# Kernel optimization log

Measured on AMD Instinct MI355X. Metric: run time of the kernel, lower is better.

The kernel has to match this reference:

```python
import jax, jax.numpy as jnp
import numpy as np

B, N, D, E = 4, 1024, 1024, 8
TOP_N = 2
THRESHOLD = 0.2
EPS = 1e-9
CAP_FACTOR = 2.0
MIN_EXPERT_CAPACITY = 4
H = int(D * 4 * 2 / 3)  # GEGLU hidden = 2730


def setup_inputs() -> dict:
    key = jax.random.key(0)
    ks = jax.random.split(key, 8)
    u = lambda k, shape, fan: jax.random.uniform(k, shape, jnp.float32, -1.0, 1.0) * (fan ** -0.5)
    return {
        "x": jax.random.normal(ks[0], (B, N, D), jnp.float32),
        "route_probs": jax.random.uniform(ks[1], (TOP_N, B, N), jnp.float32),
        "gate_w": u(ks[2], (D, E), D),
        "w1": u(ks[3], (E, D, 2 * H), 2 * H),
        "b1": u(ks[4], (E, 2 * H), 2 * H),
        "mult_bias": jnp.ones((E, H), jnp.float32),
        "w2": u(ks[5], (E, H, D), D),
        "b2": u(ks[6], (E, D), D),
    }


def reference(x, route_probs, gate_w, w1, b1, mult_bias, w2, b2):
    b, n, d = x.shape
    e = gate_w.shape[1]
    cap = max(min(n, int(n * CAP_FACTOR / e)), MIN_EXPERT_CAPACITY)  # 256

    # ---- top-n gating ----
    logits = jnp.einsum('bnd,de->bne', x, gate_w)
    raw_gates = jax.nn.softmax(logits, axis=-1)
    gate_vals, gate_idx = jax.lax.top_k(raw_gates, TOP_N)          # [b,n,k]
    gate_vals = jnp.moveaxis(gate_vals, -1, 0)                      # [k,b,n]
    gate_idx = jnp.moveaxis(gate_idx, -1, 0)                        # [k,b,n]
    one_hot_idx = jax.nn.one_hot(gate_idx, e, dtype=x.dtype)        # [k,b,n,e]

    denom = jnp.clip(gate_vals.sum(axis=0, keepdims=True), EPS)
    gate_vals = gate_vals / denom

    # route to expert k>0 with prob min(1, gate/threshold); expert 0 always routed
    should_route = route_probs < (gate_vals / THRESHOLD)
    should_route = should_route.at[0].set(True)
    mask = one_hot_idx * should_route[..., None].astype(x.dtype)    # [k,b,n,e]

    # exclusive cumsum over sequence dim -> position within each expert
    mask_cumsum = jnp.cumsum(mask, axis=2) - mask                   # [k,b,n,e]

    positions, masks = [], []
    prev_count = jnp.zeros((b, 1, e), x.dtype)
    for k in range(TOP_N):  # small fixed loop over top-n
        pos_e = (mask_cumsum[k] + prev_count) * mask[k]             # [b,n,e]
        mk = mask[k] * (pos_e < float(cap)).astype(x.dtype)
        prev_count = prev_count + mk.sum(axis=1, keepdims=True)
        positions.append(pos_e.sum(axis=-1))                        # [b,n]
        masks.append(mk)
    positions = jnp.stack(positions)                                # [k,b,n]
    mask = jnp.stack(masks)                                         # [k,b,n,e]

    mask_flat = mask.sum(axis=-1)                                   # [k,b,n] in {0,1}
    gates = gate_vals * mask_flat
    pos_one_hot = jax.nn.one_hot(positions.astype(jnp.int32), cap, dtype=x.dtype)  # [k,b,n,c]

    # combine tensor [b,n,e,c]; dispatch is its boolean support
    combine = jnp.einsum('kbn,kbne,kbnc->bnec', gates * mask_flat, one_hot_idx, pos_one_hot)
    dispatch = (combine > 0).astype(x.dtype)

    # ---- dispatch tokens to experts ----
    xe = jnp.einsum('bnd,bnec->ebcd', x, dispatch)                  # [e,b,c,d]

    # ---- per-expert GEGLU FFN (grouped GEMM) ----
    h = jnp.einsum('ebcd,edf->ebcf', xe, w1) + b1[:, None, None, :]
    val, gate = jnp.split(h, 2, axis=-1)
    act = jax.nn.gelu(gate, approximate=False) * val * mult_bias[:, None, None, :]
    out_e = jnp.einsum('ebch,ehd->ebcd', act, w2) + b2[:, None, None, :]

    # ---- combine ----
    out = jnp.einsum('ebcd,bnec->bnd', out_e, combine)
    return out


if __name__ == '__main__':
    inp = setup_inputs()
    o = reference(**inp)
    print(o.shape, o.dtype)
```

## Files before the change

kernel.cpp:

```cpp
#include <hip/hip_runtime.h>
#include <hip/hip_bf16.h>
#include <math.h>

#define B_ 4
#define N_ 1024
#define D_ 1024
#define E_ 8
#define H_ 2730
#define H2_ 5460
#define CAP_ 256
#define NTOK 4096
#define NSLOT 8192
#define NKT1 16
#define NKT2 43
#define NFG 22

typedef __attribute__((ext_vector_type(8))) short short8;
typedef __attribute__((ext_vector_type(4))) float f32x4;

__device__ __forceinline__ unsigned short f2bf(float f) {
    __hip_bfloat16 h = __float2bfloat16(f);
    return *reinterpret_cast<unsigned short*>(&h);
}
__device__ __forceinline__ float bf2f(unsigned short u) {
    unsigned x = ((unsigned)u) << 16;
    union { unsigned u; float f; } c; c.u = x; return c.f;
}

#define GLL16(g, l)                                                          \
    __builtin_amdgcn_global_load_lds(                                        \
        (const __attribute__((address_space(1))) void*)(g),                  \
        (__attribute__((address_space(3))) void*)(l), 16, 0, 0)

#define VMCNT4() asm volatile("s_waitcnt vmcnt(4)" ::: "memory")
#define VMCNT3() asm volatile("s_waitcnt vmcnt(3)" ::: "memory")
#define VMCNT0() asm volatile("s_waitcnt vmcnt(0)" ::: "memory")
#define SBAR()   __builtin_amdgcn_s_barrier()
#define SCHEDB() __builtin_amdgcn_sched_barrier(0)
#define MFMA16(a, b, c) __builtin_amdgcn_mfma_f32_16x16x32_bf16((a), (b), (c), 0, 0, 0)


__global__ __launch_bounds__(256) void k_cvt1(const float* __restrict__ w1,
                                              unsigned short* __restrict__ w1p) {
    const int fg = blockIdx.x;
    const int kt = blockIdx.y;
    const int e  = blockIdx.z;
    const float* w1e = w1 + (size_t)e * D_ * H2_;
    unsigned short* dst = w1p + (((size_t)((e * NFG + fg) * NKT1 + kt)) << 14);
    __shared__ unsigned short tile[128][66];
    const int t = threadIdx.x;
    const int fl4 = (t & 31) * 4;
    const int kr  = t >> 5;
    const int fbase = fg * 128;

    for (int m = 0; m < 2; ++m) {
        if (m) __syncthreads();
        const int c0 = m * H_;
#pragma unroll
        for (int ii = 0; ii < 8; ++ii) {
            const int kl = ii * 8 + kr;
            const float* src = w1e + (size_t)(kt * 64 + kl) * H2_ + c0 + fbase + fl4;
            float v0, v1, v2, v3;
            if (fbase + fl4 + 3 < H_) {
                const float4 v = *reinterpret_cast<const float4*>(src);
                v0 = v.x; v1 = v.y; v2 = v.z; v3 = v.w;
            } else {
                v0 = (fbase + fl4 + 0 < H_) ? src[0] : 0.f;
                v1 = (fbase + fl4 + 1 < H_) ? src[1] : 0.f;
                v2 = (fbase + fl4 + 2 < H_) ? src[2] : 0.f;
                v3 = (fbase + fl4 + 3 < H_) ? src[3] : 0.f;
            }
            tile[fl4 + 0][kl] = f2bf(v0);
            tile[fl4 + 1][kl] = f2bf(v1);
            tile[fl4 + 2][kl] = f2bf(v2);
            tile[fl4 + 3][kl] = f2bf(v3);
        }
        __syncthreads();
#pragma unroll
        for (int i = 0; i < 4; ++i) {
            const int o = i * 256 + t;
            const int k32  = o >> 9;
            const int flhi = (o >> 6) & 7;
            const int lane = o & 63;
            const int kq   = lane >> 4;
            const int fl   = flhi * 16 + (lane & 15);
            const int kb   = k32 * 32 + kq * 8;
            const unsigned* rp = reinterpret_cast<const unsigned*>(&tile[fl][kb]);
            uint4 q; q.x = rp[0]; q.y = rp[1]; q.z = rp[2]; q.w = rp[3];
            const size_t off = ((size_t)k32 << 13) + (size_t)(m * 8 + flhi) * 512 + (size_t)lane * 8;
            *reinterpret_cast<uint4*>(dst + off) = q;
        }
    }
}

__global__ __launch_bounds__(256) void k_cvt2(const float* __restrict__ w2,
                                              unsigned short* __restrict__ w2p) {
    const int kt = blockIdx.x;
    const int nt = blockIdx.y;
    const int e  = blockIdx.z;
    const float* w2e = w2 + (size_t)e * H_ * D_;
    unsigned short* dst = w2p + (((size_t)((e * 8 + nt) * NKT2 + kt)) << 13);
    __shared__ unsigned short tile[128][66];
    const int t = threadIdx.x;
    const int d4 = (t & 31) * 4;
    const int fr = t >> 5;

#pragma unroll
    for (int ii = 0; ii < 8; ++ii) {
        const int fl = ii * 8 + fr;
        const int f = kt * 64 + fl;
        float v0 = 0.f, v1 = 0.f, v2 = 0.f, v3 = 0.f;
        if (f < H_) {
            const float4 v = *reinterpret_cast<const float4*>(w2e + (size_t)f * D_ + nt * 128 + d4);
            v0 = v.x; v1 = v.y; v2 = v.z; v3 = v.w;
        }
        tile[d4 + 0][fl] = f2bf(v0);
        tile[d4 + 1][fl] = f2bf(v1);
        tile[d4 + 2][fl] = f2bf(v2);
        tile[d4 + 3][fl] = f2bf(v3);
    }
    __syncthreads();
#pragma unroll
    for (int i = 0; i < 4; ++i) {
        const int o = i * 256 + t;
        const int k32 = o >> 9;
        const int dhi = (o >> 6) & 7;
        const int lane = o & 63;
        const int kq = lane >> 4;
        const int dl = dhi * 16 + (lane & 15);
        const int fb = k32 * 32 + kq * 8;
        const unsigned* rp = reinterpret_cast<const unsigned*>(&tile[dl][fb]);
        uint4 q; q.x = rp[0]; q.y = rp[1]; q.z = rp[2]; q.w = rp[3];
        const size_t off = ((size_t)k32 << 12) + (size_t)dhi * 512 + (size_t)lane * 8;
        *reinterpret_cast<uint4*>(dst + off) = q;
    }
}

__global__ __launch_bounds__(256) void k_gate(const float* __restrict__ x,
                                              const float* __restrict__ route,
                                              const float* __restrict__ gw,
                                              int* __restrict__ tokE,
                                              float* __restrict__ tokG,
                                              int* __restrict__ tokR) {
    const int wave = threadIdx.x >> 6, lane = threadIdx.x & 63;
    const int t = blockIdx.x * 4 + wave;
    float acc[E_];
#pragma unroll
    for (int e = 0; e < E_; ++e) acc[e] = 0.f;
    const float* xr = x + (size_t)t * D_;
    for (int d = lane; d < D_; d += 64) {
        float xv = xr[d];
        const float* g = gw + d * E_;
#pragma unroll
        for (int e = 0; e < E_; ++e) acc[e] = fmaf(xv, g[e], acc[e]);
    }
#pragma unroll
    for (int e = 0; e < E_; ++e) {
#pragma unroll
        for (int off = 32; off; off >>= 1) acc[e] += __shfl_xor(acc[e], off);
    }
    if (lane == 0) {
        float m = acc[0];
#pragma unroll
        for (int e = 1; e < E_; ++e) m = fmaxf(m, acc[e]);
        float p[E_]; float s = 0.f;
#pragma unroll
        for (int e = 0; e < E_; ++e) { p[e] = expf(acc[e] - m); s += p[e]; }
        int i0 = 0; float v0 = p[0];
#pragma unroll
        for (int e = 1; e < E_; ++e) if (p[e] > v0) { v0 = p[e]; i0 = e; }
        int i1 = (i0 == 0) ? 1 : 0; float v1 = p[i1];
#pragma unroll
        for (int e = 0; e < E_; ++e) if (e != i0 && p[e] > v1) { v1 = p[e]; i1 = e; }
        float p0 = v0 / s, p1 = v1 / s;
        float denom = fmaxf(p0 + p1, 1e-9f);
        float g0 = p0 / denom, g1 = p1 / denom;
        int r1 = route[NTOK + t] < (g1 / 0.2f);
        tokE[t] = i0; tokE[NTOK + t] = i1;
        tokG[t] = g0; tokG[NTOK + t] = g1;
        tokR[t] = r1;
    }
}

__global__ __launch_bounds__(256) void k_pos(const int* __restrict__ tokE,
                                             const float* __restrict__ tokG,
                                             const int* __restrict__ tokR,
                                             int* __restrict__ sot,
                                             int* __restrict__ tos) {
    const int e = blockIdx.x & 7, b = blockIdx.x >> 3;
    const int t = threadIdx.x;
    __shared__ int sc[256];
    const int base_bt = b * N_ + t * 4;
    int m0[4], m1[4];
    int c0 = 0, c1 = 0;
#pragma unroll
    for (int i = 0; i < 4; ++i) {
        int bt = base_bt + i;
        m0[i] = (tokE[bt] == e) ? 1 : 0;
        m1[i] = ((tokE[NTOK + bt] == e) && tokR[bt]) ? 1 : 0;
        c0 += m0[i]; c1 += m1[i];
    }
    int packed = c0 | (c1 << 16);
    sc[t] = packed;
    __syncthreads();
    for (int off = 1; off < 256; off <<= 1) {
        int v = (t >= off) ? sc[t - off] : 0;
        __syncthreads();
        sc[t] += v;
        __syncthreads();
    }
    int incl = sc[t];
    int total = sc[255];
    int excl = incl - packed;
    int base0 = excl & 0xffff;
    int base1 = excl >> 16;
    int kept0 = min(total & 0xffff, CAP_);
#pragma unroll
    for (int i = 0; i < 4; ++i) {
        int bt = base_bt + i;
        if (m0[i]) {
            int pos = base0++;
            if (pos < CAP_ && tokG[bt] > 0.f) {
                int s = ((e * B_ + b) << 8) + pos;
                sot[bt] = s;
                tos[s] = bt;
            }
        }
        if (m1[i]) {
            int pos = (base1++) + kept0;
            if (pos < CAP_ && tokG[NTOK + bt] > 0.f) {
                int s = ((e * B_ + b) << 8) + pos;
                sot[NTOK + bt] = s;
                tos[s] = bt;
            }
        }
    }
}

__global__ __launch_bounds__(256) void k_disp(const float* __restrict__ x,
                                              const int* __restrict__ tos,
                                              unsigned short* __restrict__ xeP) {
    const int t = threadIdx.x;
    const int s = blockIdx.x * 2 + (t >> 7);
    const int q = t & 127;
    const int bt = tos[s];
    const int kt = q >> 3, k32 = (q >> 2) & 1, kq = q & 3;
    const int lane = (kq << 4) | (s & 15);
    const int m16 = (s >> 4) & 15;
    const int sgrp = s >> 8;
    unsigned short* dst = xeP + (((size_t)(sgrp * NKT1 + kt)) << 14) + (k32 << 13) + (m16 << 9) + lane * 8;
    ushort4 r0 = {0, 0, 0, 0}, r1 = {0, 0, 0, 0};
    if (bt >= 0) {
        const float4 v0 = *reinterpret_cast<const float4*>(x + ((size_t)bt << 10) + q * 8);
        const float4 v1 = *reinterpret_cast<const float4*>(x + ((size_t)bt << 10) + q * 8 + 4);
        r0.x = f2bf(v0.x); r0.y = f2bf(v0.y); r0.z = f2bf(v0.z); r0.w = f2bf(v0.w);
        r1.x = f2bf(v1.x); r1.y = f2bf(v1.y); r1.z = f2bf(v1.z); r1.w = f2bf(v1.w);
    }
    *reinterpret_cast<ushort4*>(dst) = r0;
    *reinterpret_cast<ushort4*>(dst + 4) = r1;
}

#define LDF(BUF, idx) (*reinterpret_cast<const short8*>(&BUF[(idx) * 512 + lane8]))

#define FFN1_MM03(AF0, AF1, AF2, AF3)                                         \
    do {                                                                      \
        acc[0][0]=MFMA16(AF0,bf0,acc[0][0]); acc[0][1]=MFMA16(AF0,bf1,acc[0][1]); \
        acc[0][2]=MFMA16(AF0,bf2,acc[0][2]); acc[0][3]=MFMA16(AF0,bf3,acc[0][3]); \
        acc[1][0]=MFMA16(AF1,bf0,acc[1][0]); acc[1][1]=MFMA16(AF1,bf1,acc[1][1]); \
        acc[1][2]=MFMA16(AF1,bf2,acc[1][2]); acc[1][3]=MFMA16(AF1,bf3,acc[1][3]); \
        acc[2][0]=MFMA16(AF2,bf0,acc[2][0]); acc[2][1]=MFMA16(AF2,bf1,acc[2][1]); \
        acc[2][2]=MFMA16(AF2,bf2,acc[2][2]); acc[2][3]=MFMA16(AF2,bf3,acc[2][3]); \
        acc[3][0]=MFMA16(AF3,bf0,acc[3][0]); acc[3][1]=MFMA16(AF3,bf1,acc[3][1]); \
        acc[3][2]=MFMA16(AF3,bf2,acc[3][2]); acc[3][3]=MFMA16(AF3,bf3,acc[3][3]); \
    } while (0)
#define FFN1_MM47(AF0, AF1, AF2, AF3)                                         \
    do {                                                                      \
        acc[4][0]=MFMA16(AF0,bf0,acc[4][0]); acc[4][1]=MFMA16(AF0,bf1,acc[4][1]); \
        acc[4][2]=MFMA16(AF0,bf2,acc[4][2]); acc[4][3]=MFMA16(AF0,bf3,acc[4][3]); \
        acc[5][0]=MFMA16(AF1,bf0,acc[5][0]); acc[5][1]=MFMA16(AF1,bf1,acc[5][1]); \
        acc[5][2]=MFMA16(AF1,bf2,acc[5][2]); acc[5][3]=MFMA16(AF1,bf3,acc[5][3]); \
        acc[6][0]=MFMA16(AF2,bf0,acc[6][0]); acc[6][1]=MFMA16(AF2,bf1,acc[6][1]); \
        acc[6][2]=MFMA16(AF2,bf2,acc[6][2]); acc[6][3]=MFMA16(AF2,bf3,acc[6][3]); \
        acc[7][0]=MFMA16(AF3,bf0,acc[7][0]); acc[7][1]=MFMA16(AF3,bf1,acc[7][1]); \
        acc[7][2]=MFMA16(AF3,bf2,acc[7][2]); acc[7][3]=MFMA16(AF3,bf3,acc[7][3]); \
    } while (0)

#define FFN1_KT(ARD, BRD, AWR, BWR, KTN, PF)                                  \
    do {                                                                      \
        const unsigned short* asn = abase + ((size_t)(KTN) << 14);            \
        const unsigned short* bsn = bbase + ((size_t)(KTN) << 14);            \
        short8 af0, af1, af2, af3, bf0, bf1, bf2, bf3;                        \
        SCHEDB(); VMCNT4(); SBAR(); SCHEDB();                                 \
        if (PF) {                                                             \
            GLL16(asn + woff + lane8, (char*)&AWR[woff]);                     \
            GLL16(asn + woff + 512 + lane8, (char*)&AWR[woff + 512]);         \
        }                                                                     \
        bf0 = LDF(BRD, bn0); bf1 = LDF(BRD, bn0 + 1);                         \
        bf2 = LDF(BRD, bn0 + 8); bf3 = LDF(BRD, bn0 + 9);                     \
        af0 = LDF(ARD, am0 + 0); af1 = LDF(ARD, am0 + 1);                     \
        af2 = LDF(ARD, am0 + 2); af3 = LDF(ARD, am0 + 3);                     \
        __builtin_amdgcn_s_setprio(1);                                        \
        FFN1_MM03(af0, af1, af2, af3);                                        \
        __builtin_amdgcn_s_setprio(0);                                        \
        if (PF) {                                                             \
            GLL16(bsn + woff + lane8, (char*)&BWR[woff]);                     \
            GLL16(bsn + woff + 512 + lane8, (char*)&BWR[woff + 512]);         \
        }                                                                     \
        af0 = LDF(ARD, am0 + 4); af1 = LDF(ARD, am0 + 5);                     \
        af2 = LDF(ARD, am0 + 6); af3 = LDF(ARD, am0 + 7);                     \
        __builtin_amdgcn_s_setprio(1);                                        \
        FFN1_MM47(af0, af1, af2, af3);                                        \
        __builtin_amdgcn_s_setprio(0);                                        \
        SCHEDB(); if (PF) { VMCNT4(); } else { VMCNT0(); } SBAR(); SCHEDB();  \
        if (PF) {                                                             \
            GLL16(asn + 8192 + woff + lane8, (char*)&AWR[8192 + woff]);       \
            GLL16(asn + 8192 + woff + 512 + lane8, (char*)&AWR[8192 + woff + 512]); \
        }                                                                     \
        bf0 = LDF(BRD, 16 + bn0); bf1 = LDF(BRD, 16 + bn0 + 1);               \
        bf2 = LDF(BRD, 16 + bn0 + 8); bf3 = LDF(BRD, 16 + bn0 + 9);           \
        af0 = LDF(ARD, 16 + am0 + 0); af1 = LDF(ARD, 16 + am0 + 1);           \
        af2 = LDF(ARD, 16 + am0 + 2); af3 = LDF(ARD, 16 + am0 + 3);           \
        __builtin_amdgcn_s_setprio(1);                                        \
        FFN1_MM03(af0, af1, af2, af3);                                        \
        __builtin_amdgcn_s_setprio(0);                                        \
        if (PF) {                                                             \
            GLL16(bsn + 8192 + woff + lane8, (char*)&BWR[8192 + woff]);       \
            GLL16(bsn + 8192 + woff + 512 + lane8, (char*)&BWR[8192 + woff + 512]); \
        }                                                                     \
        af0 = LDF(ARD, 16 + am0 + 4); af1 = LDF(ARD, 16 + am0 + 5);           \
        af2 = LDF(ARD, 16 + am0 + 6); af3 = LDF(ARD, 16 + am0 + 7);           \
        __builtin_amdgcn_s_setprio(1);                                        \
        FFN1_MM47(af0, af1, af2, af3);                                        \
        __builtin_amdgcn_s_setprio(0);                                        \
    } while (0)

__global__ __launch_bounds__(512) void k_ffn1(const unsigned short* __restrict__ xeP,
                                              const unsigned short* __restrict__ w1p,
                                              const float* __restrict__ b1,
                                              const float* __restrict__ mbias,
                                              unsigned short* __restrict__ actP) {
    const int wg = blockIdx.x;
    const int e = wg & 7;
    const int rem = wg >> 3;
    const int fg = rem >> 2;
    const int rt = rem & 3;
    const int sgrp = e * 4 + rt;

    __shared__ unsigned short Ab0[16384];
    __shared__ unsigned short Bb0[16384];
    __shared__ unsigned short Ab1[16384];
    __shared__ unsigned short Bb1[16384];

    const int tid = threadIdx.x, lane = tid & 63, w = tid >> 6;
    const int wm = w >> 2, wn = w & 3;
    const int lane8 = lane * 8;
    const int woff = w * 1024;
    const int am0 = wm * 8, bn0 = wn * 2;

    const unsigned short* abase = xeP + ((size_t)(sgrp * NKT1) << 14);
    const unsigned short* bbase = w1p + ((size_t)((e * NFG + fg) * NKT1) << 14);

    f32x4 acc[8][4];
#pragma unroll
    for (int i = 0; i < 8; ++i)
#pragma unroll
        for (int j = 0; j < 4; ++j) acc[i][j] = (f32x4)(0.f);

    GLL16(abase + woff + lane8, (char*)&Ab0[woff]);
    GLL16(abase + woff + 512 + lane8, (char*)&Ab0[woff + 512]);
    GLL16(bbase + woff + lane8, (char*)&Bb0[woff]);
    GLL16(bbase + woff + 512 + lane8, (char*)&Bb0[woff + 512]);
    GLL16(abase + 8192 + woff + lane8, (char*)&Ab0[8192 + woff]);
    GLL16(abase + 8192 + woff + 512 + lane8, (char*)&Ab0[8192 + woff + 512]);
    GLL16(bbase + 8192 + woff + lane8, (char*)&Bb0[8192 + woff]);
    GLL16(bbase + 8192 + woff + 512 + lane8, (char*)&Bb0[8192 + woff + 512]);

    for (int kt = 0; kt < NKT1; kt += 2) {
        FFN1_KT(Ab0, Bb0, Ab1, Bb1, kt + 1, 1);
        FFN1_KT(Ab1, Bb1, Ab0, Bb0, kt + 2, (kt + 2) < NKT1);
    }

    const float* b1e = b1 + (size_t)e * H2_;
    const float* mbe = mbias + (size_t)e * H_;
    const int colL = lane & 15, rq4 = (lane >> 4) * 4;
#pragma unroll
    for (int mi = 0; mi < 8; ++mi) {
        const int Rl = wm * 128 + mi * 16 + rq4;
#pragma unroll
        for (int vi = 0; vi < 2; ++vi) {
            const int f = fg * 128 + wn * 32 + vi * 16 + colL;
            if (f >= NKT2 * 64) continue;
            const bool real = f < H_;
            const float bv = real ? b1e[f] : 0.f;
            const float bg = real ? b1e[H_ + f] : 0.f;
            const float mv = real ? mbe[f] : 0.f;
            const int ktf = f >> 6, k32f = (f >> 5) & 1;
            const int lhi = ((f >> 3) & 3) << 4;
            const int bb = f & 7;
            const size_t cbase = ((size_t)(sgrp * NKT2 + ktf) << 14) + (k32f << 13);
#pragma unroll
            for (int j = 0; j < 4; ++j) {
                const int R = Rl + j;
                float a = 0.f;
                if (real) {
                    const float val = acc[mi][vi][j] + bv;
                    const float gt  = acc[mi][2 + vi][j] + bg;
                    a = 0.5f * gt * (1.f + erff(gt * 0.70710678118654752f)) * val * mv;
                }
                actP[cbase + ((R >> 4) << 9) + (size_t)((lhi | (R & 15)) * 8 + bb)] = f2bf(a);
            }
        }
    }
}

#define FFN2_MM03(AF0, AF1, AF2, AF3)                                         \
    do {                                                                      \
        acc[0][0]=MFMA16(AF0,bf0,acc[0][0]); acc[0][1]=MFMA16(AF0,bf1,acc[0][1]); \
        acc[1][0]=MFMA16(AF1,bf0,acc[1][0]); acc[1][1]=MFMA16(AF1,bf1,acc[1][1]); \
        acc[2][0]=MFMA16(AF2,bf0,acc[2][0]); acc[2][1]=MFMA16(AF2,bf1,acc[2][1]); \
        acc[3][0]=MFMA16(AF3,bf0,acc[3][0]); acc[3][1]=MFMA16(AF3,bf1,acc[3][1]); \
    } while (0)
#define FFN2_MM47(AF0, AF1, AF2, AF3)                                         \
    do {                                                                      \
        acc[4][0]=MFMA16(AF0,bf0,acc[4][0]); acc[4][1]=MFMA16(AF0,bf1,acc[4][1]); \
        acc[5][0]=MFMA16(AF1,bf0,acc[5][0]); acc[5][1]=MFMA16(AF1,bf1,acc[5][1]); \
        acc[6][0]=MFMA16(AF2,bf0,acc[6][0]); acc[6][1]=MFMA16(AF2,bf1,acc[6][1]); \
        acc[7][0]=MFMA16(AF3,bf0,acc[7][0]); acc[7][1]=MFMA16(AF3,bf1,acc[7][1]); \
    } while (0)

#define FFN2_KT(ARD, BRD, AWR, BWR, KTN, PF)                                  \
    do {                                                                      \
        const unsigned short* asn = abase + ((size_t)(KTN) << 14);            \
        const unsigned short* bsn = bbase + ((size_t)(KTN) << 13);            \
        short8 af0, af1, af2, af3, bf0, bf1;                                  \
        SCHEDB(); VMCNT3(); SBAR(); SCHEDB();                                 \
        if (PF) {                                                             \
            GLL16(asn + woff + lane8, (char*)&AWR[woff]);                     \
            GLL16(asn + woff + 512 + lane8, (char*)&AWR[woff + 512]);         \
        }                                                                     \
        bf0 = LDF(BRD, bn0); bf1 = LDF(BRD, bn0 + 1);                         \
        af0 = LDF(ARD, am0 + 0); af1 = LDF(ARD, am0 + 1);                     \
        af2 = LDF(ARD, am0 + 2); af3 = LDF(ARD, am0 + 3);                     \
        __builtin_amdgcn_s_setprio(1);                                        \
        FFN2_MM03(af0, af1, af2, af3);                                        \
        __builtin_amdgcn_s_setprio(0);                                        \
        if (PF) { GLL16(bsn + woffb + lane8, (char*)&BWR[woffb]); }           \
        af0 = LDF(ARD, am0 + 4); af1 = LDF(ARD, am0 + 5);                     \
        af2 = LDF(ARD, am0 + 6); af3 = LDF(ARD, am0 + 7);                     \
        __builtin_amdgcn_s_setprio(1);                                        \
        FFN2_MM47(af0, af1, af2, af3);                                        \
        __builtin_amdgcn_s_setprio(0);                                        \
        SCHEDB(); if (PF) { VMCNT3(); } else { VMCNT0(); } SBAR(); SCHEDB();  \
        if (PF) {                                                             \
            GLL16(asn + 8192 + woff + lane8, (char*)&AWR[8192 + woff]);       \
            GLL16(asn + 8192 + woff + 512 + lane8, (char*)&AWR[8192 + woff + 512]); \
        }                                                                     \
        bf0 = LDF(BRD, 8 + bn0); bf1 = LDF(BRD, 8 + bn0 + 1);                 \
        af0 = LDF(ARD, 16 + am0 + 0); af1 = LDF(ARD, 16 + am0 + 1);           \
        af2 = LDF(ARD, 16 + am0 + 2); af3 = LDF(ARD, 16 + am0 + 3);           \
        __builtin_amdgcn_s_setprio(1);                                        \
        FFN2_MM03(af0, af1, af2, af3);                                        \
        __builtin_amdgcn_s_setprio(0);                                        \
        if (PF) { GLL16(bsn + 4096 + woffb + lane8, (char*)&BWR[4096 + woffb]); } \
        af0 = LDF(ARD, 16 + am0 + 4); af1 = LDF(ARD, 16 + am0 + 5);           \
        af2 = LDF(ARD, 16 + am0 + 6); af3 = LDF(ARD, 16 + am0 + 7);           \
        __builtin_amdgcn_s_setprio(1);                                        \
        FFN2_MM47(af0, af1, af2, af3);                                        \
        __builtin_amdgcn_s_setprio(0);                                        \
    } while (0)

__global__ __launch_bounds__(512) void k_ffn2(const unsigned short* __restrict__ actP,
                                              const unsigned short* __restrict__ w2p,
                                              const float* __restrict__ b2,
                                              unsigned short* __restrict__ oute) {
    const int wg = blockIdx.x;
    const int e = wg & 7;
    const int rem = wg >> 3;
    const int nt = rem >> 2;
    const int mt = rem & 3;
    const int sgrp = e * 4 + mt;

    __shared__ unsigned short Ab0[16384];
    __shared__ unsigned short Bb0[8192];
    __shared__ unsigned short Ab1[16384];
    __shared__ unsigned short Bb1[8192];

    const int tid = threadIdx.x, lane = tid & 63, w = tid >> 6;
    const int wm = w >> 2, wn = w & 3;
    const int lane8 = lane * 8;
    const int woff = w * 1024;
    const int woffb = w * 512;
    const int am0 = wm * 8, bn0 = wn * 2;

    const unsigned short* abase = actP + ((size_t)(sgrp * NKT2) << 14);
    const unsigned short* bbase = w2p + ((size_t)((e * 8 + nt) * NKT2) << 13);

    f32x4 acc[8][2];
#pragma unroll
    for (int i = 0; i < 8; ++i)
#pragma unroll
        for (int j = 0; j < 2; ++j) acc[i][j] = (f32x4)(0.f);

    GLL16(abase + woff + lane8, (char*)&Ab0[woff]);
    GLL16(abase + woff + 512 + lane8, (char*)&Ab0[woff + 512]);
    GLL16(bbase + woffb + lane8, (char*)&Bb0[woffb]);
    GLL16(abase + 8192 + woff + lane8, (char*)&Ab0[8192 + woff]);
    GLL16(abase + 8192 + woff + 512 + lane8, (char*)&Ab0[8192 + woff + 512]);
    GLL16(bbase + 4096 + woffb + lane8, (char*)&Bb0[4096 + woffb]);

    for (int kt = 0; kt < NKT2 - 1; kt += 2) {
        FFN2_KT(Ab0, Bb0, Ab1, Bb1, kt + 1, 1);
        FFN2_KT(Ab1, Bb1, Ab0, Bb0, kt + 2, (kt + 2) < NKT2);
    }
    FFN2_KT(Ab0, Bb0, Ab1, Bb1, NKT2, 0);

    const float* b2e = b2 + (size_t)e * D_;
    const int colL = lane & 15, rq4 = (lane >> 4) * 4;
#pragma unroll
    for (int mi = 0; mi < 8; ++mi) {
#pragma unroll
        for (int vi = 0; vi < 2; ++vi) {
            const int d = nt * 128 + wn * 32 + vi * 16 + colL;
            const float bb2 = b2e[d];
#pragma unroll
            for (int j = 0; j < 4; ++j) {
                const int R = mt * 256 + wm * 128 + mi * 16 + rq4 + j;
                oute[((size_t)(e * 1024 + R) << 10) + d] = f2bf(acc[mi][vi][j] + bb2);
            }
        }
    }
}

__global__ __launch_bounds__(256) void k_comb(const unsigned short* __restrict__ oute,
                                              const int* __restrict__ sot,
                                              const float* __restrict__ tokG,
                                              float* __restrict__ out) {
    const int bt = blockIdx.x;
    const int t = threadIdx.x;
    const int s0 = sot[bt], s1 = sot[NTOK + bt];
    const float g0 = tokG[bt], g1 = tokG[NTOK + bt];
    float r0 = 0.f, r1 = 0.f, r2 = 0.f, r3 = 0.f;
    if (s0 >= 0) {
        const ushort4 v = *reinterpret_cast<const ushort4*>(oute + ((size_t)s0 << 10) + t * 4);
        r0 += g0 * bf2f(v.x); r1 += g0 * bf2f(v.y); r2 += g0 * bf2f(v.z); r3 += g0 * bf2f(v.w);
    }
    if (s1 >= 0) {
        const ushort4 v = *reinterpret_cast<const ushort4*>(oute + ((size_t)s1 << 10) + t * 4);
        r0 += g1 * bf2f(v.x); r1 += g1 * bf2f(v.y); r2 += g1 * bf2f(v.z); r3 += g1 * bf2f(v.w);
    }
    float4 o; o.x = r0; o.y = r1; o.z = r2; o.w = r3;
    *reinterpret_cast<float4*>(out + ((size_t)bt << 10) + t * 4) = o;
}

extern "C" void kernel_launch(void* const* d_in, const int* in_sizes, int n_in,
                              void* d_out, int out_size, void* d_ws, size_t ws_size,
                              hipStream_t stream) {
    const float* x     = (const float*)d_in[0];
    const float* route = (const float*)d_in[1];
    const float* gw    = (const float*)d_in[2];
    const float* w1    = (const float*)d_in[3];
    const float* b1    = (const float*)d_in[4];
    const float* mb    = (const float*)d_in[5];
    const float* w2    = (const float*)d_in[6];
    const float* b2    = (const float*)d_in[7];
    float* out = (float*)d_out;

    char* ws = (char*)d_ws;
    int*   tokE = (int*)(ws + 0);
    float* tokG = (float*)(ws + 32768);
    int*   tokR = (int*)(ws + 65536);
    int*   sot  = (int*)(ws + 81920);
    int*   tos  = (int*)(ws + 114688);
    unsigned short* xeP  = (unsigned short*)(ws + 147456);
    unsigned short* actP = (unsigned short*)(ws + 16924672);
    unsigned short* w1p  = (unsigned short*)(ws + 62013440);
    unsigned short* w2p  = (unsigned short*)(ws + 62013440);
    unsigned short* oute = (unsigned short*)(ws + 107102208);

    hipMemsetAsync(sot, 0xFF, 65536, stream);

    k_cvt1<<<dim3(NFG, NKT1, 8), 256, 0, stream>>>(w1, w1p);
    k_gate<<<NTOK / 4, 256, 0, stream>>>(x, route, gw, tokE, tokG, tokR);
    k_pos<<<E_ * B_, 256, 0, stream>>>(tokE, tokG, tokR, sot, tos);
    k_disp<<<NSLOT / 2, 256, 0, stream>>>(x, tos, xeP);
    k_ffn1<<<704, 512, 0, stream>>>(xeP, w1p, b1, mb, actP);
    k_cvt2<<<dim3(NKT2, 8, 8), 256, 0, stream>>>(w2, w2p);
    k_ffn2<<<256, 512, 0, stream>>>(actP, w2p, b2, oute);
    k_comb<<<NTOK, 256, 0, stream>>>(oute, sot, tokG, out);
}
```

Measured before the change: 302.3 us.

## Load GEMM fragments directly from global into registers, drop LDS staging

The FFN1 and FFN2 grouped GEMMs no longer stage tiles through LDS with global_load_lds, barriers and waitcnt. Each wave now loads its pre-swizzled MFMA fragments straight from global memory into registers, software-pipelined in two register sets. The memset of the slot map is folded into the gating and position kernels, and gating weights are read as float4. This removes LDS traffic and barrier syncs but raises register pressure and loses sharing of tiles across waves, so each wave fetches data that other waves also fetch, leaning on the cache.

```diff
diff --git a/kernel.cpp b/kernel.cpp
--- a/kernel.cpp
+++ b/kernel.cpp
@@ -27,17 +27,8 @@
     union { unsigned u; float f; } c; c.u = x; return c.f;
 }
 
-#define GLL16(g, l)                                                          \
-    __builtin_amdgcn_global_load_lds(                                        \
-        (const __attribute__((address_space(1))) void*)(g),                  \
-        (__attribute__((address_space(3))) void*)(l), 16, 0, 0)
-
-#define VMCNT4() asm volatile("s_waitcnt vmcnt(4)" ::: "memory")
-#define VMCNT3() asm volatile("s_waitcnt vmcnt(3)" ::: "memory")
-#define VMCNT0() asm volatile("s_waitcnt vmcnt(0)" ::: "memory")
-#define SBAR()   __builtin_amdgcn_s_barrier()
-#define SCHEDB() __builtin_amdgcn_sched_barrier(0)
 #define MFMA16(a, b, c) __builtin_amdgcn_mfma_f32_16x16x32_bf16((a), (b), (c), 0, 0, 0)
+#define LD8(p) (*reinterpret_cast<const short8*>(p))
 
 
 __global__ __launch_bounds__(256) void k_cvt1(const float* __restrict__ w1,
@@ -141,7 +132,8 @@
                                               const float* __restrict__ gw,
                                               int* __restrict__ tokE,
                                               float* __restrict__ tokG,
-                                              int* __restrict__ tokR) {
+                                              int* __restrict__ tokR,
+                                              int* __restrict__ sot) {
     const int wave = threadIdx.x >> 6, lane = threadIdx.x & 63;
     const int t = blockIdx.x * 4 + wave;
     float acc[E_];
@@ -149,10 +141,13 @@
     for (int e = 0; e < E_; ++e) acc[e] = 0.f;
     const float* xr = x + (size_t)t * D_;
     for (int d = lane; d < D_; d += 64) {
-        float xv = xr[d];
-        const float* g = gw + d * E_;
-#pragma unroll
-        for (int e = 0; e < E_; ++e) acc[e] = fmaf(xv, g[e], acc[e]);
+        const float xv = xr[d];
+        const float4 g0 = *reinterpret_cast<const float4*>(gw + d * 8);
+        const float4 g1 = *reinterpret_cast<const float4*>(gw + d * 8 + 4);
+        acc[0] = fmaf(xv, g0.x, acc[0]); acc[1] = fmaf(xv, g0.y, acc[1]);
+        acc[2] = fmaf(xv, g0.z, acc[2]); acc[3] = fmaf(xv, g0.w, acc[3]);
+        acc[4] = fmaf(xv, g1.x, acc[4]); acc[5] = fmaf(xv, g1.y, acc[5]);
+        acc[6] = fmaf(xv, g1.z, acc[6]); acc[7] = fmaf(xv, g1.w, acc[7]);
     }
 #pragma unroll
     for (int e = 0; e < E_; ++e) {
@@ -179,6 +174,7 @@
         tokE[t] = i0; tokE[NTOK + t] = i1;
         tokG[t] = g0; tokG[NTOK + t] = g1;
         tokR[t] = r1;
+        sot[t] = -1; sot[NTOK + t] = -1;
     }
 }
 
@@ -190,6 +186,7 @@
     const int e = blockIdx.x & 7, b = blockIdx.x >> 3;
     const int t = threadIdx.x;
     __shared__ int sc[256];
+    tos[((e * B_ + b) << 8) + t] = -1;
     const int base_bt = b * N_ + t * 4;
     int m0[4], m1[4];
     int c0 = 0, c1 = 0;
@@ -260,77 +257,37 @@
     *reinterpret_cast<ushort4*>(dst + 4) = r1;
 }
 
-#define LDF(BUF, idx) (*reinterpret_cast<const short8*>(&BUF[(idx) * 512 + lane8]))
-
-#define FFN1_MM03(AF0, AF1, AF2, AF3)                                         \
+#define LOADG1(P, G)                                                          \
     do {                                                                      \
-        acc[0][0]=MFMA16(AF0,bf0,acc[0][0]); acc[0][1]=MFMA16(AF0,bf1,acc[0][1]); \
-        acc[0][2]=MFMA16(AF0,bf2,acc[0][2]); acc[0][3]=MFMA16(AF0,bf3,acc[0][3]); \
-        acc[1][0]=MFMA16(AF1,bf0,acc[1][0]); acc[1][1]=MFMA16(AF1,bf1,acc[1][1]); \
-        acc[1][2]=MFMA16(AF1,bf2,acc[1][2]); acc[1][3]=MFMA16(AF1,bf3,acc[1][3]); \
-        acc[2][0]=MFMA16(AF2,bf0,acc[2][0]); acc[2][1]=MFMA16(AF2,bf1,acc[2][1]); \
-        acc[2][2]=MFMA16(AF2,bf2,acc[2][2]); acc[2][3]=MFMA16(AF2,bf3,acc[2][3]); \
-        acc[3][0]=MFMA16(AF3,bf0,acc[3][0]); acc[3][1]=MFMA16(AF3,bf1,acc[3][1]); \
-        acc[3][2]=MFMA16(AF3,bf2,acc[3][2]); acc[3][3]=MFMA16(AF3,bf3,acc[3][3]); \
+        const unsigned short* ap = aw + (size_t)(G) * 8192;                   \
+        const unsigned short* bp = bw + (size_t)(G) * 8192;                   \
+        P##A0 = LD8(ap);        P##A1 = LD8(ap + 512);                        \
+        P##A2 = LD8(ap + 1024); P##A3 = LD8(ap + 1536);                       \
+        P##A4 = LD8(ap + 2048); P##A5 = LD8(ap + 2560);                       \
+        P##A6 = LD8(ap + 3072); P##A7 = LD8(ap + 3584);                       \
+        P##V0 = LD8(bp);        P##V1 = LD8(bp + 512);                        \
+        P##G0 = LD8(bp + 4096); P##G1 = LD8(bp + 4608);                       \
     } while (0)
-#define FFN1_MM47(AF0, AF1, AF2, AF3)                                         \
+
+#define MFMAG1(P)                                                             \
     do {                                                                      \
-        acc[4][0]=MFMA16(AF0,bf0,acc[4][0]); acc[4][1]=MFMA16(AF0,bf1,acc[4][1]); \
-        acc[4][2]=MFMA16(AF0,bf2,acc[4][2]); acc[4][3]=MFMA16(AF0,bf3,acc[4][3]); \
-        acc[5][0]=MFMA16(AF1,bf0,acc[5][0]); acc[5][1]=MFMA16(AF1,bf1,acc[5][1]); \
-        acc[5][2]=MFMA16(AF1,bf2,acc[5][2]); acc[5][3]=MFMA16(AF1,bf3,acc[5][3]); \
-        acc[6][0]=MFMA16(AF2,bf0,acc[6][0]); acc[6][1]=MFMA16(AF2,bf1,acc[6][1]); \
-        acc[6][2]=MFMA16(AF2,bf2,acc[6][2]); acc[6][3]=MFMA16(AF2,bf3,acc[6][3]); \
-        acc[7][0]=MFMA16(AF3,bf0,acc[7][0]); acc[7][1]=MFMA16(AF3,bf1,acc[7][1]); \
-        acc[7][2]=MFMA16(AF3,bf2,acc[7][2]); acc[7][3]=MFMA16(AF3,bf3,acc[7][3]); \
-    } while (0)
-
-#define FFN1_KT(ARD, BRD, AWR, BWR, KTN, PF)                                  \
-    do {                                                                      \
-        const unsigned short* asn = abase + ((size_t)(KTN) << 14);            \
-        const unsigned short* bsn = bbase + ((size_t)(KTN) << 14);            \
-        short8 af0, af1, af2, af3, bf0, bf1, bf2, bf3;                        \
-        SCHEDB(); VMCNT4(); SBAR(); SCHEDB();                                 \
-        if (PF) {                                                             \
-            GLL16(asn + woff + lane8, (char*)&AWR[woff]);                     \
-            GLL16(asn + woff + 512 + lane8, (char*)&AWR[woff + 512]);         \
-        }                                                                     \
-        bf0 = LDF(BRD, bn0); bf1 = LDF(BRD, bn0 + 1);                         \
-        bf2 = LDF(BRD, bn0 + 8); bf3 = LDF(BRD, bn0 + 9);                     \
-        af0 = LDF(ARD, am0 + 0); af1 = LDF(ARD, am0 + 1);                     \
-        af2 = LDF(ARD, am0 + 2); af3 = LDF(ARD, am0 + 3);                     \
         __builtin_amdgcn_s_setprio(1);                                        \
-        FFN1_MM03(af0, af1, af2, af3);                                        \
-        __builtin_amdgcn_s_setprio(0);                                        \
-        if (PF) {                                                             \
-            GLL16(bsn + woff + lane8, (char*)&BWR[woff]);                     \
-            GLL16(bsn + woff + 512 + lane8, (char*)&BWR[woff + 512]);         \
-        }                                                                     \
-        af0 = LDF(ARD, am0 + 4); af1 = LDF(ARD, am0 + 5);                     \
-        af2 = LDF(ARD, am0 + 6); af3 = LDF(ARD, am0 + 7);                     \
-        __builtin_amdgcn_s_setprio(1);                                        \
-        FFN1_MM47(af0, af1, af2, af3);                                        \
-        __builtin_amdgcn_s_setprio(0);                                        \
-        SCHEDB(); if (PF) { VMCNT4(); } else { VMCNT0(); } SBAR(); SCHEDB();  \
-        if (PF) {                                                             \
-            GLL16(asn + 8192 + woff + lane8, (char*)&AWR[8192 + woff]);       \
-            GLL16(asn + 8192 + woff + 512 + lane8, (char*)&AWR[8192 + woff + 512]); \
-        }                                                                     \
-        bf0 = LDF(BRD, 16 + bn0); bf1 = LDF(BRD, 16 + bn0 + 1);               \
-        bf2 = LDF(BRD, 16 + bn0 + 8); bf3 = LDF(BRD, 16 + bn0 + 9);           \
-        af0 = LDF(ARD, 16 + am0 + 0); af1 = LDF(ARD, 16 + am0 + 1);           \
-        af2 = LDF(ARD, 16 + am0 + 2); af3 = LDF(ARD, 16 + am0 + 3);           \
-        __builtin_amdgcn_s_setprio(1);                                        \
-        FFN1_MM03(af0, af1, af2, af3);                                        \
-        __builtin_amdgcn_s_setprio(0);                                        \
-        if (PF) {                                                             \
-            GLL16(bsn + 8192 + woff + lane8, (char*)&BWR[8192 + woff]);       \
-            GLL16(bsn + 8192 + woff + 512 + lane8, (char*)&BWR[8192 + woff + 512]); \
-        }                                                                     \
-        af0 = LDF(ARD, 16 + am0 + 4); af1 = LDF(ARD, 16 + am0 + 5);           \
-        af2 = LDF(ARD, 16 + am0 + 6); af3 = LDF(ARD, 16 + am0 + 7);           \
-        __builtin_amdgcn_s_setprio(1);                                        \
-        FFN1_MM47(af0, af1, af2, af3);                                        \
+        acc[0][0]=MFMA16(P##A0,P##V0,acc[0][0]); acc[0][1]=MFMA16(P##A0,P##V1,acc[0][1]); \
+        acc[0][2]=MFMA16(P##A0,P##G0,acc[0][2]); acc[0][3]=MFMA16(P##A0,P##G1,acc[0][3]); \
+        acc[1][0]=MFMA16(P##A1,P##V0,acc[1][0]); acc[1][1]=MFMA16(P##A1,P##V1,acc[1][1]); \
+        acc[1][2]=MFMA16(P##A1,P##G0,acc[1][2]); acc[1][3]=MFMA16(P##A1,P##G1,acc[1][3]); \
+        acc[2][0]=MFMA16(P##A2,P##V0,acc[2][0]); acc[2][1]=MFMA16(P##A2,P##V1,acc[2][1]); \
+        acc[2][2]=MFMA16(P##A2,P##G0,acc[2][2]); acc[2][3]=MFMA16(P##A2,P##G1,acc[2][3]); \
+        acc[3][0]=MFMA16(P##A3,P##V0,acc[3][0]); acc[3][1]=MFMA16(P##A3,P##V1,acc[3][1]); \
+        acc[3][2]=MFMA16(P##A3,P##G0,acc[3][2]); acc[3][3]=MFMA16(P##A3,P##G1,acc[3][3]); \
+        acc[4][0]=MFMA16(P##A4,P##V0,acc[4][0]); acc[4][1]=MFMA16(P##A4,P##V1,acc[4][1]); \
+        acc[4][2]=MFMA16(P##A4,P##G0,acc[4][2]); acc[4][3]=MFMA16(P##A4,P##G1,acc[4][3]); \
+        acc[5][0]=MFMA16(P##A5,P##V0,acc[5][0]); acc[5][1]=MFMA16(P##A5,P##V1,acc[5][1]); \
+        acc[5][2]=MFMA16(P##A5,P##G0,acc[5][2]); acc[5][3]=MFMA16(P##A5,P##G1,acc[5][3]); \
+        acc[6][0]=MFMA16(P##A6,P##V0,acc[6][0]); acc[6][1]=MFMA16(P##A6,P##V1,acc[6][1]); \
+        acc[6][2]=MFMA16(P##A6,P##G0,acc[6][2]); acc[6][3]=MFMA16(P##A6,P##G1,acc[6][3]); \
+        acc[7][0]=MFMA16(P##A7,P##V0,acc[7][0]); acc[7][1]=MFMA16(P##A7,P##V1,acc[7][1]); \
+        acc[7][2]=MFMA16(P##A7,P##G0,acc[7][2]); acc[7][3]=MFMA16(P##A7,P##G1,acc[7][3]); \
         __builtin_amdgcn_s_setprio(0);                                        \
     } while (0)
 
@@ -346,19 +303,12 @@
     const int rt = rem & 3;
     const int sgrp = e * 4 + rt;
 
-    __shared__ unsigned short Ab0[16384];
-    __shared__ unsigned short Bb0[16384];
-    __shared__ unsigned short Ab1[16384];
-    __shared__ unsigned short Bb1[16384];
-
     const int tid = threadIdx.x, lane = tid & 63, w = tid >> 6;
     const int wm = w >> 2, wn = w & 3;
     const int lane8 = lane * 8;
-    const int woff = w * 1024;
-    const int am0 = wm * 8, bn0 = wn * 2;
-
-    const unsigned short* abase = xeP + ((size_t)(sgrp * NKT1) << 14);
-    const unsigned short* bbase = w1p + ((size_t)((e * NFG + fg) * NKT1) << 14);
+
+    const unsigned short* aw = xeP + ((size_t)(sgrp * NKT1) << 14) + (wm * 8) * 512 + lane8;
+    const unsigned short* bw = w1p + ((size_t)((e * NFG + fg) * NKT1) << 14) + (wn * 2) * 512 + lane8;
 
     f32x4 acc[8][4];
 #pragma unroll
@@ -366,18 +316,15 @@
 #pragma unroll
         for (int j = 0; j < 4; ++j) acc[i][j] = (f32x4)(0.f);
 
-    GLL16(abase + woff + lane8, (char*)&Ab0[woff]);
-    GLL16(abase + woff + 512 + lane8, (char*)&Ab0[woff + 512]);
-    GLL16(bbase + woff + lane8, (char*)&Bb0[woff]);
-    GLL16(bbase + woff + 512 + lane8, (char*)&Bb0[woff + 512]);
-    GLL16(abase + 8192 + woff + lane8, (char*)&Ab0[8192 + woff]);
-    GLL16(abase + 8192 + woff + 512 + lane8, (char*)&Ab0[8192 + woff + 512]);
-    GLL16(bbase + 8192 + woff + lane8, (char*)&Bb0[8192 + woff]);
-    GLL16(bbase + 8192 + woff + 512 + lane8, (char*)&Bb0[8192 + woff + 512]);
-
-    for (int kt = 0; kt < NKT1; kt += 2) {
-        FFN1_KT(Ab0, Bb0, Ab1, Bb1, kt + 1, 1);
-        FFN1_KT(Ab1, Bb1, Ab0, Bb0, kt + 2, (kt + 2) < NKT1);
+    short8 cA0, cA1, cA2, cA3, cA4, cA5, cA6, cA7, cV0, cV1, cG0, cG1;
+    short8 nA0, nA1, nA2, nA3, nA4, nA5, nA6, nA7, nV0, nV1, nG0, nG1;
+
+    LOADG1(c, 0);
+    for (int g = 0; g < 32; g += 2) {
+        LOADG1(n, g + 1);
+        MFMAG1(c);
+        if (g + 2 < 32) LOADG1(c, g + 2);
+        MFMAG1(n);
     }
 
     const float* b1e = b1 + (size_t)e * H2_;
@@ -413,59 +360,28 @@
     }
 }
 
-#define FFN2_MM03(AF0, AF1, AF2, AF3)                                         \
+#define LOADG2(P, G)                                                          \
     do {                                                                      \
-        acc[0][0]=MFMA16(AF0,bf0,acc[0][0]); acc[0][1]=MFMA16(AF0,bf1,acc[0][1]); \
-        acc[1][0]=MFMA16(AF1,bf0,acc[1][0]); acc[1][1]=MFMA16(AF1,bf1,acc[1][1]); \
-        acc[2][0]=MFMA16(AF2,bf0,acc[2][0]); acc[2][1]=MFMA16(AF2,bf1,acc[2][1]); \
-        acc[3][0]=MFMA16(AF3,bf0,acc[3][0]); acc[3][1]=MFMA16(AF3,bf1,acc[3][1]); \
+        const unsigned short* ap = aw + (size_t)(G) * 8192;                   \
+        const unsigned short* bp = bw + (size_t)(G) * 4096;                   \
+        P##A0 = LD8(ap);        P##A1 = LD8(ap + 512);                        \
+        P##A2 = LD8(ap + 1024); P##A3 = LD8(ap + 1536);                       \
+        P##A4 = LD8(ap + 2048); P##A5 = LD8(ap + 2560);                       \
+        P##A6 = LD8(ap + 3072); P##A7 = LD8(ap + 3584);                       \
+        P##B0 = LD8(bp);        P##B1 = LD8(bp + 512);                        \
     } while (0)
-#define FFN2_MM47(AF0, AF1, AF2, AF3)                                         \
+
+#define MFMAG2(P)                                                             \
     do {                                                                      \
-        acc[4][0]=MFMA16(AF0,bf0,acc[4][0]); acc[4][1]=MFMA16(AF0,bf1,acc[4][1]); \
-        acc[5][0]=MFMA16(AF1,bf0,acc[5][0]); acc[5][1]=MFMA16(AF1,bf1,acc[5][1]); \
-        acc[6][0]=MFMA16(AF2,bf0,acc[6][0]); acc[6][1]=MFMA16(AF2,bf1,acc[6][1]); \
-        acc[7][0]=MFMA16(AF3,bf0,acc[7][0]); acc[7][1]=MFMA16(AF3,bf1,acc[7][1]); \
-    } while (0)
-
-#define FFN2_KT(ARD, BRD, AWR, BWR, KTN, PF)                                  \
-    do {                                                                      \
-        const unsigned short* asn = abase + ((size_t)(KTN) << 14);            \
-        const unsigned short* bsn = bbase + ((size_t)(KTN) << 13);            \
-        short8 af0, af1, af2, af3, bf0, bf1;                                  \
-        SCHEDB(); VMCNT3(); SBAR(); SCHEDB();                                 \
-        if (PF) {                                                             \
-            GLL16(asn + woff + lane8, (char*)&AWR[woff]);                     \
-            GLL16(asn + woff + 512 + lane8, (char*)&AWR[woff + 512]);         \
-        }                                                                     \
-        bf0 = LDF(BRD, bn0); bf1 = LDF(BRD, bn0 + 1);                         \
-        af0 = LDF(ARD, am0 + 0); af1 = LDF(ARD, am0 + 1);                     \
-        af2 = LDF(ARD, am0 + 2); af3 = LDF(ARD, am0 + 3);                     \
         __builtin_amdgcn_s_setprio(1);                                        \
-        FFN2_MM03(af0, af1, af2, af3);                                        \
-        __builtin_amdgcn_s_setprio(0);                                        \
-        if (PF) { GLL16(bsn + woffb + lane8, (char*)&BWR[woffb]); }           \
-        af0 = LDF(ARD, am0 + 4); af1 = LDF(ARD, am0 + 5);                     \
-        af2 = LDF(ARD, am0 + 6); af3 = LDF(ARD, am0 + 7);                     \
-        __builtin_amdgcn_s_setprio(1);                                        \
-        FFN2_MM47(af0, af1, af2, af3);                                        \
-        __builtin_amdgcn_s_setprio(0);                                        \
-        SCHEDB(); if (PF) { VMCNT3(); } else { VMCNT0(); } SBAR(); SCHEDB();  \
-        if (PF) {                                                             \
-            GLL16(asn + 8192 + woff + lane8, (char*)&AWR[8192 + woff]);       \
-            GLL16(asn + 8192 + woff + 512 + lane8, (char*)&AWR[8192 + woff + 512]); \
-        }                                                                     \
-        bf0 = LDF(BRD, 8 + bn0); bf1 = LDF(BRD, 8 + bn0 + 1);                 \
-        af0 = LDF(ARD, 16 + am0 + 0); af1 = LDF(ARD, 16 + am0 + 1);           \
-        af2 = LDF(ARD, 16 + am0 + 2); af3 = LDF(ARD, 16 + am0 + 3);           \
-        __builtin_amdgcn_s_setprio(1);                                        \
-        FFN2_MM03(af0, af1, af2, af3);                                        \
-        __builtin_amdgcn_s_setprio(0);                                        \
-        if (PF) { GLL16(bsn + 4096 + woffb + lane8, (char*)&BWR[4096 + woffb]); } \
-        af0 = LDF(ARD, 16 + am0 + 4); af1 = LDF(ARD, 16 + am0 + 5);           \
-        af2 = LDF(ARD, 16 + am0 + 6); af3 = LDF(ARD, 16 + am0 + 7);           \
-        __builtin_amdgcn_s_setprio(1);                                        \
-        FFN2_MM47(af0, af1, af2, af3);                                        \
+        acc[0][0]=MFMA16(P##A0,P##B0,acc[0][0]); acc[0][1]=MFMA16(P##A0,P##B1,acc[0][1]); \
+        acc[1][0]=MFMA16(P##A1,P##B0,acc[1][0]); acc[1][1]=MFMA16(P##A1,P##B1,acc[1][1]); \
+        acc[2][0]=MFMA16(P##A2,P##B0,acc[2][0]); acc[2][1]=MFMA16(P##A2,P##B1,acc[2][1]); \
+        acc[3][0]=MFMA16(P##A3,P##B0,acc[3][0]); acc[3][1]=MFMA16(P##A3,P##B1,acc[3][1]); \
+        acc[4][0]=MFMA16(P##A4,P##B0,acc[4][0]); acc[4][1]=MFMA16(P##A4,P##B1,acc[4][1]); \
+        acc[5][0]=MFMA16(P##A5,P##B0,acc[5][0]); acc[5][1]=MFMA16(P##A5,P##B1,acc[5][1]); \
+        acc[6][0]=MFMA16(P##A6,P##B0,acc[6][0]); acc[6][1]=MFMA16(P##A6,P##B1,acc[6][1]); \
+        acc[7][0]=MFMA16(P##A7,P##B0,acc[7][0]); acc[7][1]=MFMA16(P##A7,P##B1,acc[7][1]); \
         __builtin_amdgcn_s_setprio(0);                                        \
     } while (0)
 
@@ -480,20 +396,12 @@
     const int mt = rem & 3;
     const int sgrp = e * 4 + mt;
 
-    __shared__ unsigned short Ab0[16384];
-    __shared__ unsigned short Bb0[8192];
-    __shared__ unsigned short Ab1[16384];
-    __shared__ unsigned short Bb1[8192];
-
     const int tid = threadIdx.x, lane = tid & 63, w = tid >> 6;
     const int wm = w >> 2, wn = w & 3;
     const int lane8 = lane * 8;
-    const int woff = w * 1024;
-    const int woffb = w * 512;
-    const int am0 = wm * 8, bn0 = wn * 2;
-
-    const unsigned short* abase = actP + ((size_t)(sgrp * NKT2) << 14);
-    const unsigned short* bbase = w2p + ((size_t)((e * 8 + nt) * NKT2) << 13);
+
+    const unsigned short* aw = actP + ((size_t)(sgrp * NKT2) << 14) + (wm * 8) * 512 + lane8;
+    const unsigned short* bw = w2p + ((size_t)((e * 8 + nt) * NKT2) << 13) + (wn * 2) * 512 + lane8;
 
     f32x4 acc[8][2];
 #pragma unroll
@@ -501,18 +409,16 @@
 #pragma unroll
         for (int j = 0; j < 2; ++j) acc[i][j] = (f32x4)(0.f);
 
-    GLL16(abase + woff + lane8, (char*)&Ab0[woff]);
-    GLL16(abase + woff + 512 + lane8, (char*)&Ab0[woff + 512]);
-    GLL16(bbase + woffb + lane8, (char*)&Bb0[woffb]);
-    GLL16(abase + 8192 + woff + lane8, (char*)&Ab0[8192 + woff]);
-    GLL16(abase + 8192 + woff + 512 + lane8, (char*)&Ab0[8192 + woff + 512]);
-    GLL16(bbase + 4096 + woffb + lane8, (char*)&Bb0[4096 + woffb]);
-
-    for (int kt = 0; kt < NKT2 - 1; kt += 2) {
-        FFN2_KT(Ab0, Bb0, Ab1, Bb1, kt + 1, 1);
-        FFN2_KT(Ab1, Bb1, Ab0, Bb0, kt + 2, (kt + 2) < NKT2);
-    }
-    FFN2_KT(Ab0, Bb0, Ab1, Bb1, NKT2, 0);
+    short8 cA0, cA1, cA2, cA3, cA4, cA5, cA6, cA7, cB0, cB1;
+    short8 nA0, nA1, nA2, nA3, nA4, nA5, nA6, nA7, nB0, nB1;
+
+    LOADG2(c, 0);
+    for (int g = 0; g < 86; g += 2) {
+        LOADG2(n, g + 1);
+        MFMAG2(c);
+        if (g + 2 < 86) LOADG2(c, g + 2);
+        MFMAG2(n);
+    }
 
     const float* b2e = b2 + (size_t)e * D_;
     const int colL = lane & 15, rq4 = (lane >> 4) * 4;
@@ -577,10 +483,8 @@
     unsigned short* w2p  = (unsigned short*)(ws + 62013440);
     unsigned short* oute = (unsigned short*)(ws + 107102208);
 
-    hipMemsetAsync(sot, 0xFF, 65536, stream);
-
     k_cvt1<<<dim3(NFG, NKT1, 8), 256, 0, stream>>>(w1, w1p);
-    k_gate<<<NTOK / 4, 256, 0, stream>>>(x, route, gw, tokE, tokG, tokR);
+    k_gate<<<NTOK / 4, 256, 0, stream>>>(x, route, gw, tokE, tokG, tokR, sot);
     k_pos<<<E_ * B_, 256, 0, stream>>>(tokE, tokG, tokR, sot, tos);
     k_disp<<<NSLOT / 2, 256, 0, stream>>>(x, tos, xeP);
     k_ffn1<<<704, 512, 0, stream>>>(xeP, w1p, b1, mb, actP);
```

Result: slower. 316.8 us (+4.8%).
